# Performance work log

Measured on AMD Instinct MI355X. Metric: run time of the kernel, lower is better.

The kernel has to match this reference:

```python
import jax, jax.numpy as jnp
import numpy as np

B, N, IN_DIM, OUT_DIM = 8, 2048, 256, 256
EDGE_P = 0.02   # adjacency density
MASK_P = 0.9    # fraction of valid nodes


def setup_inputs() -> dict:
    key = jax.random.key(0)
    ks = jax.random.split(key, 8)
    x = jax.random.normal(ks[0], (B, N, IN_DIM), dtype=jnp.float32)
    adj = (jax.random.uniform(ks[1], (B, N, N)) < EDGE_P).astype(jnp.float32)
    mask = (jax.random.uniform(ks[2], (B, N)) < MASK_P).astype(jnp.float32)
    # nn.Linear(in_dim, out_dim): W [out, in], b [out]
    lim1 = 1.0 / np.sqrt(IN_DIM)
    W = jax.random.uniform(ks[3], (OUT_DIM, IN_DIM), minval=-lim1, maxval=lim1, dtype=jnp.float32)
    b = jax.random.uniform(ks[4], (OUT_DIM,), minval=-lim1, maxval=lim1, dtype=jnp.float32)
    # nn.Linear(2*out_dim, 1): weight [1, 2D] split into a1 (acts on h_i), a2 (acts on h_j)
    lim2 = 1.0 / np.sqrt(2 * OUT_DIM)
    a1 = jax.random.uniform(ks[5], (OUT_DIM,), minval=-lim2, maxval=lim2, dtype=jnp.float32)
    a2 = jax.random.uniform(ks[6], (OUT_DIM,), minval=-lim2, maxval=lim2, dtype=jnp.float32)
    att_b = jax.random.uniform(ks[7], (), minval=-lim2, maxval=lim2, dtype=jnp.float32)
    return {"x": x, "adj": adj, "mask": mask, "W": W, "b": b, "a1": a1, "a2": a2, "att_b": att_b}


def reference(x, adj, mask, W, b, a1, a2, att_b):
    # h = Linear(x): [B, N, D]
    h = jnp.einsum('bni,di->bnd', x, W) + b
    # attention(cat([h_i, h_j])) == h_i @ a1 + h_j @ a2 + att_b (linear in each half)
    s1 = h @ a1  # [B, N] -> contributes along i
    s2 = h @ a2  # [B, N] -> contributes along j
    logits = s1[:, :, None] + s2[:, None, :] + att_b  # [B, N, N]
    att = jax.nn.sigmoid(logits) * adj
    att = att * mask[:, :, None] * mask[:, None, :]
    att = att / (jnp.sum(att, axis=-1, keepdims=True) + 1e-8)
    h_new = jnp.einsum('bij,bjd->bid', att, h)
    return h_new * mask[:, :, None]
```

## Files before the change

### kernel.cpp

```cpp
#include <hip/hip_runtime.h>
#include <hip/hip_bf16.h>

#define BB 8
#define NN 2048
#define DD 256
#define MM (BB * NN)

typedef __attribute__((ext_vector_type(8))) short bf16x8_t;
typedef __attribute__((ext_vector_type(4))) float f32x4_t;

__global__ __launch_bounds__(256) void gemm_h(
    const float* __restrict__ x,
    const float* __restrict__ Wt,
    const float* __restrict__ bias,
    __hip_bfloat16* __restrict__ h)
{
    __shared__ __hip_bfloat16 As[64][72];
    __shared__ __hip_bfloat16 Bs[64][72];

    const int tid  = threadIdx.x;
    const int r    = tid >> 2;
    const int cs   = (tid & 3) * 16;
    const int w    = tid >> 6;
    const int lane = tid & 63;
    const int m16  = lane & 15;
    const int quad = lane >> 4;
    const long rowBase = (long)blockIdx.x * 64;
    const int  colBase = blockIdx.y * 64;

    f32x4_t acc[4];
#pragma unroll
    for (int c = 0; c < 4; c++) acc[c] = (f32x4_t){0.f, 0.f, 0.f, 0.f};

    for (int k0 = 0; k0 < 256; k0 += 64) {
        const float4* ag = (const float4*)(x  + (rowBase + r) * 256 + k0 + cs);
        const float4* bg = (const float4*)(Wt + (long)(colBase + r) * 256 + k0 + cs);
        float4 av[4], bv[4];
#pragma unroll
        for (int q = 0; q < 4; q++) { av[q] = ag[q]; bv[q] = bg[q]; }

        __align__(16) __hip_bfloat16 ta[16], tb[16];
#pragma unroll
        for (int q = 0; q < 4; q++) {
            ta[q * 4 + 0] = __float2bfloat16(av[q].x);
            ta[q * 4 + 1] = __float2bfloat16(av[q].y);
            ta[q * 4 + 2] = __float2bfloat16(av[q].z);
            ta[q * 4 + 3] = __float2bfloat16(av[q].w);
            tb[q * 4 + 0] = __float2bfloat16(bv[q].x);
            tb[q * 4 + 1] = __float2bfloat16(bv[q].y);
            tb[q * 4 + 2] = __float2bfloat16(bv[q].z);
            tb[q * 4 + 3] = __float2bfloat16(bv[q].w);
        }

        __syncthreads();
        *(uint4*)&As[r][cs]     = *(uint4*)&ta[0];
        *(uint4*)&As[r][cs + 8] = *(uint4*)&ta[8];
        *(uint4*)&Bs[r][cs]     = *(uint4*)&tb[0];
        *(uint4*)&Bs[r][cs + 8] = *(uint4*)&tb[8];
        __syncthreads();

#pragma unroll
        for (int kk = 0; kk < 64; kk += 32) {
            bf16x8_t af = *(const bf16x8_t*)&As[w * 16 + m16][kk + quad * 8];
#pragma unroll
            for (int c = 0; c < 4; c++) {
                bf16x8_t bf = *(const bf16x8_t*)&Bs[c * 16 + m16][kk + quad * 8];
                acc[c] = __builtin_amdgcn_mfma_f32_16x16x32_bf16(af, bf, acc[c], 0, 0, 0);
            }
        }
    }

#pragma unroll
    for (int c = 0; c < 4; c++) {
        const int col = colBase + c * 16 + m16;
        const float bv = bias[col];
#pragma unroll
        for (int reg = 0; reg < 4; reg++) {
            const long row = rowBase + w * 16 + quad * 4 + reg;
            h[row * 256 + col] = __float2bfloat16(acc[c][reg] + bv);
        }
    }
}

struct __attribute__((aligned(8))) bf4 { __hip_bfloat16 v[4]; };

__global__ __launch_bounds__(256) void s_kernel(
    const __hip_bfloat16* __restrict__ h,
    const float* __restrict__ a1,
    const float* __restrict__ a2,
    float* __restrict__ s1, float* __restrict__ s2)
{
    const int w = threadIdx.x >> 6;
    const int lane = threadIdx.x & 63;
    const long row = (long)blockIdx.x * 4 + w;

    bf4 hv = *(const bf4*)(h + row * 256 + lane * 4);
    float4 A1 = *(const float4*)(a1 + lane * 4);
    float4 A2 = *(const float4*)(a2 + lane * 4);
    float p1 = 0.f, p2 = 0.f;
    const float h0 = __bfloat162float(hv.v[0]), h1 = __bfloat162float(hv.v[1]);
    const float h2 = __bfloat162float(hv.v[2]), h3 = __bfloat162float(hv.v[3]);
    p1 = h0 * A1.x + h1 * A1.y + h2 * A1.z + h3 * A1.w;
    p2 = h0 * A2.x + h1 * A2.y + h2 * A2.z + h3 * A2.w;
#pragma unroll
    for (int off = 32; off; off >>= 1) {
        p1 += __shfl_down(p1, off);
        p2 += __shfl_down(p2, off);
    }
    if (lane == 0) { s1[row] = p1; s2[row] = p2; }
}

__global__ __launch_bounds__(256) void attn_agg(
    const float* __restrict__ adj,
    const float* __restrict__ mask,
    const __hip_bfloat16* __restrict__ h,
    const float* __restrict__ s1,
    const float* __restrict__ s2,
    const float* __restrict__ attb_p,
    float* __restrict__ out)
{
    __shared__ unsigned short s_j[2048];
    __shared__ float s_w[2048];
    __shared__ int   s_cnt;
    __shared__ float s_red[4];
    __shared__ float s_inv;

    const int tid = threadIdx.x;
    const int b   = blockIdx.x & 7;
    const int i   = blockIdx.x >> 3;
    const long row = (long)b * NN + i;

    const float mask_i = mask[row];
    if (mask_i == 0.f) {
        out[row * 256 + tid] = 0.f;
        return;
    }
    if (tid == 0) s_cnt = 0;
    __syncthreads();

    const float si = s1[row] + attb_p[0];
    const long mbase = (long)b * NN;

    const float4* arow = (const float4*)(adj + row * NN);
    float4 A0 = arow[tid * 2];
    float4 A1 = arow[tid * 2 + 1];
    float av[8] = {A0.x, A0.y, A0.z, A0.w, A1.x, A1.y, A1.z, A1.w};
    float lsum = 0.f;
#pragma unroll
    for (int e = 0; e < 8; e++) {
        if (av[e] != 0.f) {
            const int j = tid * 8 + e;
            const float mj = mask[mbase + j];
            if (mj != 0.f) {
                const float z = si + s2[mbase + j];
                const float wgt = av[e] * mj / (1.f + __expf(-z));
                const int pos = atomicAdd(&s_cnt, 1);
                s_j[pos] = (unsigned short)j;
                s_w[pos] = wgt;
                lsum += wgt;
            }
        }
    }

#pragma unroll
    for (int off = 32; off; off >>= 1) lsum += __shfl_down(lsum, off);
    const int lane = tid & 63, w = tid >> 6;
    if (lane == 0) s_red[w] = lsum;
    __syncthreads();
    if (tid == 0) {
        const float t = s_red[0] + s_red[1] + s_red[2] + s_red[3];
        s_inv = 1.f / (t + 1e-8f);
    }
    __syncthreads();

    const int cnt = s_cnt;
    const float inv = s_inv;
    const __hip_bfloat16* hb = h + mbase * 256 + tid;
    float acc = 0.f;
    int k = 0;
    for (; k + 4 <= cnt; k += 4) {
        const int j0 = s_j[k], j1 = s_j[k + 1], j2 = s_j[k + 2], j3 = s_j[k + 3];
        const float w0 = s_w[k], w1 = s_w[k + 1], w2 = s_w[k + 2], w3 = s_w[k + 3];
        const float g0 = __bfloat162float(hb[(long)j0 * 256]);
        const float g1 = __bfloat162float(hb[(long)j1 * 256]);
        const float g2 = __bfloat162float(hb[(long)j2 * 256]);
        const float g3 = __bfloat162float(hb[(long)j3 * 256]);
        acc += w0 * g0 + w1 * g1 + w2 * g2 + w3 * g3;
    }
    for (; k < cnt; k++)
        acc += s_w[k] * __bfloat162float(hb[(long)s_j[k] * 256]);

    out[row * 256 + tid] = acc * inv;
}

extern "C" void kernel_launch(void* const* d_in, const int* in_sizes, int n_in,
                              void* d_out, int out_size, void* d_ws, size_t ws_size,
                              hipStream_t stream) {
    const float* x    = (const float*)d_in[0];
    const float* adj  = (const float*)d_in[1];
    const float* mask = (const float*)d_in[2];
    const float* W    = (const float*)d_in[3];
    const float* bias = (const float*)d_in[4];
    const float* a1   = (const float*)d_in[5];
    const float* a2   = (const float*)d_in[6];
    const float* attb = (const float*)d_in[7];
    float* out = (float*)d_out;

    __hip_bfloat16* h = (__hip_bfloat16*)d_ws;
    float* s1 = (float*)((char*)d_ws + (size_t)MM * DD * 2);
    float* s2 = s1 + MM;

    gemm_h<<<dim3(MM / 64, DD / 64), 256, 0, stream>>>(x, W, bias, h);
    s_kernel<<<MM / 4, 256, 0, stream>>>(h, a1, a2, s1, s2);
    attn_agg<<<MM, 256, 0, stream>>>(adj, mask, h, s1, s2, attb, out);
}
```

Before: 257.3 us.

## Process two attention rows per block with packed bf16x2 gathers

The aggregation kernel now handles two query rows per 256-thread block, 128 threads per row. Each thread gathers a 32-bit word holding two bf16 features instead of one 16-bit value, and writes a float2. The adjacency row is read with coalesced float4 loads across four strided passes. The aim is fewer blocks, wider memory transactions and half as many gather instructions per feature. The cost is that masked rows no longer exit early; those threads still sit through the block barriers and write zeros.

```diff
diff --git a/kernel.cpp b/kernel.cpp
--- a/kernel.cpp
+++ b/kernel.cpp
@@ -97,11 +97,10 @@
     bf4 hv = *(const bf4*)(h + row * 256 + lane * 4);
     float4 A1 = *(const float4*)(a1 + lane * 4);
     float4 A2 = *(const float4*)(a2 + lane * 4);
-    float p1 = 0.f, p2 = 0.f;
     const float h0 = __bfloat162float(hv.v[0]), h1 = __bfloat162float(hv.v[1]);
     const float h2 = __bfloat162float(hv.v[2]), h3 = __bfloat162float(hv.v[3]);
-    p1 = h0 * A1.x + h1 * A1.y + h2 * A1.z + h3 * A1.w;
-    p2 = h0 * A2.x + h1 * A2.y + h2 * A2.z + h3 * A2.w;
+    float p1 = h0 * A1.x + h1 * A1.y + h2 * A1.z + h3 * A1.w;
+    float p2 = h0 * A2.x + h1 * A2.y + h2 * A2.z + h3 * A2.w;
 #pragma unroll
     for (int off = 32; off; off >>= 1) {
         p1 += __shfl_down(p1, off);
@@ -119,78 +118,92 @@
     const float* __restrict__ attb_p,
     float* __restrict__ out)
 {
-    __shared__ unsigned short s_j[2048];
-    __shared__ float s_w[2048];
-    __shared__ int   s_cnt;
-    __shared__ float s_red[4];
-    __shared__ float s_inv;
-
-    const int tid = threadIdx.x;
-    const int b   = blockIdx.x & 7;
-    const int i   = blockIdx.x >> 3;
+    __shared__ unsigned short s_j[2][2048];
+    __shared__ float s_w[2][2048];
+    __shared__ int   s_cnt[2];
+    __shared__ float s_red[2][2];
+    __shared__ float s_inv[2];
+
+    const int tid  = threadIdx.x;
+    const int half = tid >> 7;
+    const int t    = tid & 127;
+    const int b    = blockIdx.x & 7;
+    const int i    = ((blockIdx.x >> 3) << 1) + half;
     const long row = (long)b * NN + i;
+    const long mbase = (long)b * NN;
 
     const float mask_i = mask[row];
-    if (mask_i == 0.f) {
-        out[row * 256 + tid] = 0.f;
-        return;
-    }
-    if (tid == 0) s_cnt = 0;
+    const bool  valid  = (mask_i != 0.f);
+
+    if (t == 0) s_cnt[half] = 0;
     __syncthreads();
 
     const float si = s1[row] + attb_p[0];
-    const long mbase = (long)b * NN;
 
     const float4* arow = (const float4*)(adj + row * NN);
-    float4 A0 = arow[tid * 2];
-    float4 A1 = arow[tid * 2 + 1];
-    float av[8] = {A0.x, A0.y, A0.z, A0.w, A1.x, A1.y, A1.z, A1.w};
     float lsum = 0.f;
 #pragma unroll
-    for (int e = 0; e < 8; e++) {
-        if (av[e] != 0.f) {
-            const int j = tid * 8 + e;
-            const float mj = mask[mbase + j];
-            if (mj != 0.f) {
-                const float z = si + s2[mbase + j];
-                const float wgt = av[e] * mj / (1.f + __expf(-z));
-                const int pos = atomicAdd(&s_cnt, 1);
-                s_j[pos] = (unsigned short)j;
-                s_w[pos] = wgt;
-                lsum += wgt;
+    for (int l = 0; l < 4; l++) {
+        float4 A = arow[l * 128 + t];
+        const int jb = l * 512 + t * 4;
+        float av[4] = {A.x, A.y, A.z, A.w};
+#pragma unroll
+        for (int e = 0; e < 4; e++) {
+            if (valid && av[e] != 0.f) {
+                const int j = jb + e;
+                const float mj = mask[mbase + j];
+                if (mj != 0.f) {
+                    const float z = si + s2[mbase + j];
+                    const float wgt = av[e] * mj / (1.f + __expf(-z));
+                    const int pos = atomicAdd(&s_cnt[half], 1);
+                    s_j[half][pos] = (unsigned short)j;
+                    s_w[half][pos] = wgt;
+                    lsum += wgt;
+                }
             }
         }
     }
 
 #pragma unroll
     for (int off = 32; off; off >>= 1) lsum += __shfl_down(lsum, off);
-    const int lane = tid & 63, w = tid >> 6;
-    if (lane == 0) s_red[w] = lsum;
+    const int lane = tid & 63;
+    if (lane == 0) s_red[half][(tid >> 6) & 1] = lsum;
     __syncthreads();
-    if (tid == 0) {
-        const float t = s_red[0] + s_red[1] + s_red[2] + s_red[3];
-        s_inv = 1.f / (t + 1e-8f);
-    }
+    if (t == 0) s_inv[half] = 1.f / (s_red[half][0] + s_red[half][1] + 1e-8f);
     __syncthreads();
 
-    const int cnt = s_cnt;
-    const float inv = s_inv;
-    const __hip_bfloat16* hb = h + mbase * 256 + tid;
-    float acc = 0.f;
+    const int cnt = s_cnt[half];
+    const float inv = s_inv[half];
+    const unsigned int* h2 = (const unsigned int*)h;
+    const unsigned int rbase = (unsigned int)(mbase)*128u + (unsigned int)t;
+    float accx = 0.f, accy = 0.f;
     int k = 0;
     for (; k + 4 <= cnt; k += 4) {
-        const int j0 = s_j[k], j1 = s_j[k + 1], j2 = s_j[k + 2], j3 = s_j[k + 3];
-        const float w0 = s_w[k], w1 = s_w[k + 1], w2 = s_w[k + 2], w3 = s_w[k + 3];
-        const float g0 = __bfloat162float(hb[(long)j0 * 256]);
-        const float g1 = __bfloat162float(hb[(long)j1 * 256]);
-        const float g2 = __bfloat162float(hb[(long)j2 * 256]);
-        const float g3 = __bfloat162float(hb[(long)j3 * 256]);
-        acc += w0 * g0 + w1 * g1 + w2 * g2 + w3 * g3;
-    }
-    for (; k < cnt; k++)
-        acc += s_w[k] * __bfloat162float(hb[(long)s_j[k] * 256]);
-
-    out[row * 256 + tid] = acc * inv;
+        ushort4 j4 = *(const ushort4*)&s_j[half][k];
+        float4  w4 = *(const float4*)&s_w[half][k];
+        unsigned int u0 = h2[rbase + (unsigned int)j4.x * 128u];
+        unsigned int u1 = h2[rbase + (unsigned int)j4.y * 128u];
+        unsigned int u2 = h2[rbase + (unsigned int)j4.z * 128u];
+        unsigned int u3 = h2[rbase + (unsigned int)j4.w * 128u];
+        accx += w4.x * __uint_as_float(u0 << 16);
+        accy += w4.x * __uint_as_float(u0 & 0xffff0000u);
+        accx += w4.y * __uint_as_float(u1 << 16);
+        accy += w4.y * __uint_as_float(u1 & 0xffff0000u);
+        accx += w4.z * __uint_as_float(u2 << 16);
+        accy += w4.z * __uint_as_float(u2 & 0xffff0000u);
+        accx += w4.w * __uint_as_float(u3 << 16);
+        accy += w4.w * __uint_as_float(u3 & 0xffff0000u);
+    }
+    for (; k < cnt; k++) {
+        const unsigned int jj = s_j[half][k];
+        const float wk = s_w[half][k];
+        unsigned int u = h2[rbase + jj * 128u];
+        accx += wk * __uint_as_float(u << 16);
+        accy += wk * __uint_as_float(u & 0xffff0000u);
+    }
+
+    float2* o2 = (float2*)(out + row * 256);
+    o2[t] = make_float2(accx * inv, accy * inv);
 }
 
 extern "C" void kernel_launch(void* const* d_in, const int* in_sizes, int n_in,
@@ -212,5 +225,5 @@
 
     gemm_h<<<dim3(MM / 64, DD / 64), 256, 0, stream>>>(x, W, bias, h);
     s_kernel<<<MM / 4, 256, 0, stream>>>(h, a1, a2, s1, s2);
-    attn_agg<<<MM, 256, 0, stream>>>(adj, mask, h, s1, s2, attb, out);
-}
+    attn_agg<<<MM / 2, 256, 0, stream>>>(adj, mask, h, s1, s2, attb, out);
+}
```

Result: slower. 295.5 us (+14.8%).
